# Optimization experiments

Measured on AMD Instinct MI355X. Metric: run time of the kernel, lower is better.

## Reference

```python
import jax, jax.numpy as jnp
import numpy as np

IN_FEATURES = 4096
OUT_FEATURES = 4096
ALPHA = 0.002
BETA = 0.01


def setup_inputs() -> dict:
    key = jax.random.key(0)
    k_x, k_w, k_b = jax.random.split(key, 3)
    # int8 activations, weights, bias (matching torch.randint(-127, 127, ...))
    x = jax.random.randint(k_x, (4, 2048, IN_FEATURES), -127, 127, dtype=jnp.int32).astype(jnp.int8)
    weight = jax.random.randint(k_w, (OUT_FEATURES, IN_FEATURES), -127, 127, dtype=jnp.int32).astype(jnp.int8)
    bias = jax.random.randint(k_b, (1, OUT_FEATURES), -127, 127, dtype=jnp.int32).astype(jnp.int8)
    a = jnp.float32(ALPHA)
    b = jnp.float32(BETA)
    return {"x": x, "weight": weight, "bias": bias, "a": a, "b": b}


def reference(x, weight, bias, a, b):
    # int8 bias add, and requantize-to-int8 epilogue.
    x_shape = x.shape
    x2d = x.reshape(-1, x_shape[-1])                       # [M, K] int8
    # int32 accumulation: acc = x @ W^T
    acc = jnp.matmul(x2d.astype(jnp.int32), weight.T.astype(jnp.int32),
                     preferred_element_type=jnp.int32)      # [M, N] int32
    # epilogue: alpha * acc + beta * bias, round + clamp to int8 range
    y = a * acc.astype(jnp.float32) + b * bias.astype(jnp.float32)
    y = jnp.clip(jnp.round(y), -128.0, 127.0).astype(jnp.int8)
    return y.reshape(*x_shape[:-1], -1)
```

## Files before the change

### kernel.cpp

```cpp
#include <hip/hip_runtime.h>

#define K_DIM 4096
#define N_DIM 4096
#define NT (K_DIM / 64)

typedef int v4i __attribute__((ext_vector_type(4)));
typedef int v16i __attribute__((ext_vector_type(16)));

__device__ __forceinline__ void gload_lds16(const void* g, void* l) {
  __builtin_amdgcn_global_load_lds(
      (const __attribute__((address_space(1))) void*)g,
      (__attribute__((address_space(3))) void*)l, 16, 0, 0);
}

__device__ __forceinline__ int pack4(int4 w) {
  return (w.x & 0xff) | ((w.y & 0xff) << 8) | ((w.z & 0xff) << 16) | (w.w << 24);
}

__global__ __launch_bounds__(256) void pack_kernel(const int* __restrict__ src,
                                                   int4* __restrict__ dst, int n16) {
  int i = blockIdx.x * 256 + threadIdx.x;
  if (i >= n16) return;
  const int4* s = (const int4*)src + (size_t)i * 4;
  int4 w0 = s[0], w1 = s[1], w2 = s[2], w3 = s[3];
  int4 r;
  r.x = pack4(w0); r.y = pack4(w1); r.z = pack4(w2); r.w = pack4(w3);
  dst[i] = r;
}

__global__ __launch_bounds__(512, 2) void gemm256(
    const char* __restrict__ Ap, const char* __restrict__ Bp,
    const int* __restrict__ bias, const float* __restrict__ pa,
    const float* __restrict__ pb, int* __restrict__ out) {
  extern __shared__ __align__(16) char lds[];

  const int tid = threadIdx.x;
  const int wid = tid >> 6;
  const int lane = tid & 63;

  const int nwg = gridDim.x;
  const int cpx = nwg >> 3;
  const int flat = blockIdx.x;
  const int wg = (flat & 7) * cpx + (flat >> 3);
  const int br = wg >> 4;
  const int bn = wg & 15;

  const int wr = wid >> 2;
  const int wcol = wid & 3;

  const int srow = tid >> 2;
  const int schunk = (tid & 3) ^ ((tid >> 3) & 3);
  const char* aSrc = Ap + (size_t)(br * 256 + srow) * K_DIM + schunk * 16;
  const char* bSrc = Bp + (size_t)(bn * 256 + srow) * K_DIM + schunk * 16;

  auto stage = [&](int kt) {
    const char* sa = aSrc + kt * 64;
    const char* sb2 = bSrc + kt * 64;
    char* da = lds + (kt & 3) * 16384 + wid * 1024;
    char* db = lds + 65536 + (kt & 3) * 16384 + wid * 1024;
    gload_lds16(sa, da);
    gload_lds16(sa + (size_t)128 * K_DIM, da + 8192);
    gload_lds16(sb2, db);
    gload_lds16(sb2 + (size_t)128 * K_DIM, db + 8192);
  };

  const int lrow = lane & 31;
  const int hi = lane >> 5;
  const int swz = (lrow >> 1) & 3;
  const int kOff0 = (hi ^ swz) << 4;
  const int kOff1 = kOff0 ^ 32;
  const int aBase = (wr * 128 + lrow) * 64;
  const int bBase = 65536 + (wcol * 64 + lrow) * 64;

  v16i acc[4][2];
  {
    v16i z = {0};
#pragma unroll
    for (int mi = 0; mi < 4; ++mi)
#pragma unroll
      for (int ni = 0; ni < 2; ++ni) acc[mi][ni] = z;
  }

  stage(0); stage(1); stage(2);
  asm volatile("s_waitcnt vmcnt(8)" ::: "memory");
  __builtin_amdgcn_s_barrier();

  for (int kt = 0; kt < NT; ++kt) {
    const int sb = (kt & 3) * 16384;

    v4i a0[4], b0[2], a1[4], b1[2];
#pragma unroll
    for (int mi = 0; mi < 4; ++mi) a0[mi] = *(const v4i*)&lds[sb + aBase + mi * 2048 + kOff0];
#pragma unroll
    for (int ni = 0; ni < 2; ++ni) b0[ni] = *(const v4i*)&lds[sb + bBase + ni * 2048 + kOff0];
#pragma unroll
    for (int mi = 0; mi < 4; ++mi) a1[mi] = *(const v4i*)&lds[sb + aBase + mi * 2048 + kOff1];
#pragma unroll
    for (int ni = 0; ni < 2; ++ni) b1[ni] = *(const v4i*)&lds[sb + bBase + ni * 2048 + kOff1];

    if (kt + 3 < NT) stage(kt + 3);

    asm volatile("s_waitcnt lgkmcnt(6)" ::: "memory");
    __builtin_amdgcn_sched_barrier(0);
    __builtin_amdgcn_s_setprio(1);
#pragma unroll
    for (int mi = 0; mi < 4; ++mi)
#pragma unroll
      for (int ni = 0; ni < 2; ++ni)
        acc[mi][ni] =
            __builtin_amdgcn_mfma_i32_32x32x32_i8(a0[mi], b0[ni], acc[mi][ni], 0, 0, 0);
    __builtin_amdgcn_s_setprio(0);

    asm volatile("s_waitcnt lgkmcnt(0)" ::: "memory");
    __builtin_amdgcn_sched_barrier(0);
    __builtin_amdgcn_s_setprio(1);
#pragma unroll
    for (int mi = 0; mi < 4; ++mi)
#pragma unroll
      for (int ni = 0; ni < 2; ++ni)
        acc[mi][ni] =
            __builtin_amdgcn_mfma_i32_32x32x32_i8(a1[mi], b1[ni], acc[mi][ni], 0, 0, 0);
    __builtin_amdgcn_s_setprio(0);

    if (kt < NT - 3)
      asm volatile("s_waitcnt vmcnt(4)" ::: "memory");
    else
      asm volatile("s_waitcnt vmcnt(0)" ::: "memory");
    __builtin_amdgcn_s_barrier();
  }

  const float alpha = *pa;
  const float beta = *pb;
#pragma unroll
  for (int ni = 0; ni < 2; ++ni) {
    const int n = bn * 256 + wcol * 64 + ni * 32 + lrow;
    const float bb = __fmul_rn(beta, (float)bias[n]);
#pragma unroll
    for (int mi = 0; mi < 4; ++mi) {
#pragma unroll
      for (int r = 0; r < 16; ++r) {
        const int row = (r & 3) + 8 * (r >> 2) + 4 * hi;
        const int m = br * 256 + wr * 128 + mi * 32 + row;
        float y = __fadd_rn(__fmul_rn(alpha, (float)acc[mi][ni][r]), bb);
        y = rintf(y);
        y = fminf(127.f, fmaxf(-128.f, y));
        out[(size_t)m * N_DIM + n] = (int)y;
      }
    }
  }
}

extern "C" void kernel_launch(void* const* d_in, const int* in_sizes, int n_in,
                              void* d_out, int out_size, void* d_ws, size_t ws_size,
                              hipStream_t stream) {
  const int* x = (const int*)d_in[0];
  const int* w = (const int*)d_in[1];
  const int* bias = (const int*)d_in[2];
  const float* pa = (const float*)d_in[3];
  const float* pb = (const float*)d_in[4];
  int* out = (int*)d_out;

  const int M = in_sizes[0] / K_DIM;
  const size_t xBytes = (size_t)M * K_DIM;
  const size_t wBytes = (size_t)N_DIM * K_DIM;

  char* xp = (char*)d_ws;
  char* wp = xp + xBytes;
  const int n16x = (int)(xBytes / 16);
  const int n16w = (int)(wBytes / 16);
  pack_kernel<<<(n16x + 255) / 256, 256, 0, stream>>>(x, (int4*)xp, n16x);
  pack_kernel<<<(n16w + 255) / 256, 256, 0, stream>>>(w, (int4*)wp, n16w);

  const int nwg = (M / 256) * (N_DIM / 256);
  hipFuncSetAttribute((const void*)gemm256,
                      hipFuncAttributeMaxDynamicSharedMemorySize, 131072);
  gemm256<<<nwg, 512, 131072, stream>>>(xp, wp, bias, pa, pb, out);
}
```

Measured before the change: 203.6 us.

## Switch GEMM pipeline to BK=128 double buffering with XOR-swizzled LDS

The main loop changes from a 4-stage ring of 64-wide K tiles to a 2-stage double buffer of 128-wide K tiles, halving the number of barriers and vmcnt waits per K. Each iteration now issues the next stage's global-to-LDS loads first, then runs four rounds of MFMA over the current buffer. LDS rows become 128 bytes with an 8-way XOR chunk swizzle to avoid bank conflicts. The cost is shallower prefetch: only one tile is in flight, and the loop waits on vmcnt(0) every iteration, so global latency may be exposed more often.

```diff
diff --git a/kernel.cpp b/kernel.cpp
--- a/kernel.cpp
+++ b/kernel.cpp
@@ -2,7 +2,7 @@
 
 #define K_DIM 4096
 #define N_DIM 4096
-#define NT (K_DIM / 64)
+#define NT (K_DIM / 128)
 
 typedef int v4i __attribute__((ext_vector_type(4)));
 typedef int v16i __attribute__((ext_vector_type(16)));
@@ -48,29 +48,32 @@
   const int wr = wid >> 2;
   const int wcol = wid & 3;
 
-  const int srow = tid >> 2;
-  const int schunk = (tid & 3) ^ ((tid >> 3) & 3);
+  const int srow = tid >> 3;
+  const int schunk = (tid & 7) ^ (srow & 7);
   const char* aSrc = Ap + (size_t)(br * 256 + srow) * K_DIM + schunk * 16;
   const char* bSrc = Bp + (size_t)(bn * 256 + srow) * K_DIM + schunk * 16;
+  char* const dA = lds + tid * 16;
+  char* const dB = lds + 65536 + tid * 16;
 
   auto stage = [&](int kt) {
-    const char* sa = aSrc + kt * 64;
-    const char* sb2 = bSrc + kt * 64;
-    char* da = lds + (kt & 3) * 16384 + wid * 1024;
-    char* db = lds + 65536 + (kt & 3) * 16384 + wid * 1024;
-    gload_lds16(sa, da);
-    gload_lds16(sa + (size_t)128 * K_DIM, da + 8192);
-    gload_lds16(sb2, db);
-    gload_lds16(sb2 + (size_t)128 * K_DIM, db + 8192);
+    const int s = (kt & 1) * 32768;
+    const char* sa = aSrc + kt * 128;
+    const char* sbp = bSrc + kt * 128;
+#pragma unroll
+    for (int j = 0; j < 4; ++j) {
+      gload_lds16(sa + (size_t)j * 64 * K_DIM, dA + s + j * 8192);
+      gload_lds16(sbp + (size_t)j * 64 * K_DIM, dB + s + j * 8192);
+    }
   };
 
   const int lrow = lane & 31;
   const int hi = lane >> 5;
-  const int swz = (lrow >> 1) & 3;
-  const int kOff0 = (hi ^ swz) << 4;
-  const int kOff1 = kOff0 ^ 32;
-  const int aBase = (wr * 128 + lrow) * 64;
-  const int bBase = 65536 + (wcol * 64 + lrow) * 64;
+  const int aBase = (wr * 128 + lrow) * 128;
+  const int bBase = 65536 + (wcol * 64 + lrow) * 128;
+  const int p0 = ((0 + hi) ^ (lrow & 7)) << 4;
+  const int p1 = ((2 + hi) ^ (lrow & 7)) << 4;
+  const int p2 = ((4 + hi) ^ (lrow & 7)) << 4;
+  const int p3 = ((6 + hi) ^ (lrow & 7)) << 4;
 
   v16i acc[4][2];
   {
@@ -81,24 +84,23 @@
       for (int ni = 0; ni < 2; ++ni) acc[mi][ni] = z;
   }
 
-  stage(0); stage(1); stage(2);
-  asm volatile("s_waitcnt vmcnt(8)" ::: "memory");
+  stage(0);
+  asm volatile("s_waitcnt vmcnt(0)" ::: "memory");
   __builtin_amdgcn_s_barrier();
 
   for (int kt = 0; kt < NT; ++kt) {
-    const int sb = (kt & 3) * 16384;
+    const int sb = (kt & 1) * 32768;
+    if (kt + 1 < NT) stage(kt + 1);
 
     v4i a0[4], b0[2], a1[4], b1[2];
 #pragma unroll
-    for (int mi = 0; mi < 4; ++mi) a0[mi] = *(const v4i*)&lds[sb + aBase + mi * 2048 + kOff0];
-#pragma unroll
-    for (int ni = 0; ni < 2; ++ni) b0[ni] = *(const v4i*)&lds[sb + bBase + ni * 2048 + kOff0];
-#pragma unroll
-    for (int mi = 0; mi < 4; ++mi) a1[mi] = *(const v4i*)&lds[sb + aBase + mi * 2048 + kOff1];
-#pragma unroll
-    for (int ni = 0; ni < 2; ++ni) b1[ni] = *(const v4i*)&lds[sb + bBase + ni * 2048 + kOff1];
-
-    if (kt + 3 < NT) stage(kt + 3);
+    for (int mi = 0; mi < 4; ++mi) a0[mi] = *(const v4i*)&lds[sb + aBase + mi * 4096 + p0];
+#pragma unroll
+    for (int ni = 0; ni < 2; ++ni) b0[ni] = *(const v4i*)&lds[sb + bBase + ni * 4096 + p0];
+#pragma unroll
+    for (int mi = 0; mi < 4; ++mi) a1[mi] = *(const v4i*)&lds[sb + aBase + mi * 4096 + p1];
+#pragma unroll
+    for (int ni = 0; ni < 2; ++ni) b1[ni] = *(const v4i*)&lds[sb + bBase + ni * 4096 + p1];
 
     asm volatile("s_waitcnt lgkmcnt(6)" ::: "memory");
     __builtin_amdgcn_sched_barrier(0);
@@ -122,11 +124,41 @@
             __builtin_amdgcn_mfma_i32_32x32x32_i8(a1[mi], b1[ni], acc[mi][ni], 0, 0, 0);
     __builtin_amdgcn_s_setprio(0);
 
-    if (kt < NT - 3)
-      asm volatile("s_waitcnt vmcnt(4)" ::: "memory");
-    else
+#pragma unroll
+    for (int mi = 0; mi < 4; ++mi) a0[mi] = *(const v4i*)&lds[sb + aBase + mi * 4096 + p2];
+#pragma unroll
+    for (int ni = 0; ni < 2; ++ni) b0[ni] = *(const v4i*)&lds[sb + bBase + ni * 4096 + p2];
+#pragma unroll
+    for (int mi = 0; mi < 4; ++mi) a1[mi] = *(const v4i*)&lds[sb + aBase + mi * 4096 + p3];
+#pragma unroll
+    for (int ni = 0; ni < 2; ++ni) b1[ni] = *(const v4i*)&lds[sb + bBase + ni * 4096 + p3];
+
+    asm volatile("s_waitcnt lgkmcnt(6)" ::: "memory");
+    __builtin_amdgcn_sched_barrier(0);
+    __builtin_amdgcn_s_setprio(1);
+#pragma unroll
+    for (int mi = 0; mi < 4; ++mi)
+#pragma unroll
+      for (int ni = 0; ni < 2; ++ni)
+        acc[mi][ni] =
+            __builtin_amdgcn_mfma_i32_32x32x32_i8(a0[mi], b0[ni], acc[mi][ni], 0, 0, 0);
+    __builtin_amdgcn_s_setprio(0);
+
+    asm volatile("s_waitcnt lgkmcnt(0)" ::: "memory");
+    __builtin_amdgcn_sched_barrier(0);
+    __builtin_amdgcn_s_setprio(1);
+#pragma unroll
+    for (int mi = 0; mi < 4; ++mi)
+#pragma unroll
+      for (int ni = 0; ni < 2; ++ni)
+        acc[mi][ni] =
+            __builtin_amdgcn_mfma_i32_32x32x32_i8(a1[mi], b1[ni], acc[mi][ni], 0, 0, 0);
+    __builtin_amdgcn_s_setprio(0);
+
+    if (kt + 1 < NT) {
       asm volatile("s_waitcnt vmcnt(0)" ::: "memory");
-    __builtin_amdgcn_s_barrier();
+      __builtin_amdgcn_s_barrier();
+    }
   }
 
   const float alpha = *pa;
```

New measurement: 197.8 us. 1.03x faster.
